# Kernel optimization log

Measured on AMD Instinct MI355X. Metric: run time of the kernel, lower is better.

The kernel has to match this reference:

```python
import jax, jax.numpy as jnp
import numpy as np

B, C, T = 16, 768, 9
S = T * T * T            # 729 tokens
H = 8                    # heads
E = 3                    # experts
HID = C * 4              # expert hidden dim (mult=4)


def setup_inputs() -> dict:
    key = jax.random.key(0)
    ks = jax.random.split(key, 8)
    w = lambda k, sh: (jax.random.normal(k, sh, jnp.float32) * 0.02)
    return {
        "x": jax.random.normal(ks[0], (B, C, T, T, T), jnp.float32),
        "ln_gamma": jnp.ones((C, T, T, T), jnp.float32),
        "ln_beta": jnp.zeros((C, T, T, T), jnp.float32),
        "w_qkv": w(ks[1], (C, 3 * C)),
        "w_out": w(ks[2], (C, C)),
        "w_gate": w(ks[3], (C, E)),
        "b_gate": jnp.zeros((E,), jnp.float32),
        "w1": w(ks[4], (E, C, HID)),
        "b1": jnp.zeros((E, HID), jnp.float32),
        "w2": w(ks[5], (E, HID, C)),
        "b2": jnp.zeros((E, C), jnp.float32),
    }


def reference(x, ln_gamma, ln_beta, w_qkv, w_out, w_gate, b_gate, w1, b1, w2, b2):
    b = x.shape[0]
    # LayerNorm over (C, T, H, W) per batch element, affine params [C,T,T,T]
    mu = jnp.mean(x, axis=(1, 2, 3, 4), keepdims=True)
    var = jnp.var(x, axis=(1, 2, 3, 4), keepdims=True)
    xn = (x - mu) * jax.lax.rsqrt(var + 1e-5) * ln_gamma + ln_beta

    # ---- attention (NOTE: source applies no 1/sqrt(d) scaling) ----
    tok = xn.reshape(b, C, S).transpose(0, 2, 1)                 # [b,s,c]
    qkv = (tok @ w_qkv).reshape(b, S, 3, H, C // H)              # [b,s,3,h,d]
    q = qkv[:, :, 0].transpose(0, 2, 1, 3)                       # [b,h,s,d]
    k = qkv[:, :, 1].transpose(0, 2, 1, 3)
    v = qkv[:, :, 2].transpose(0, 2, 1, 3)
    attn = jax.nn.softmax(jnp.einsum('bhqd,bhkd->bhqk', q, k), axis=-1)
    ctx = jnp.einsum('bhqk,bhkd->bqhd', attn, v).reshape(b, S, C)
    attn_out = (ctx @ w_out).transpose(0, 2, 1).reshape(b, C, T, T, T)
    x2 = x + attn_out                                            # residual (dropout = eval identity)

    # ---- switch-MoE (top-1 gate, all experts computed densely then masked) ----
    tok2 = x2.reshape(b, C, S).transpose(0, 2, 1)                # [b,s,c]
    gate = jax.nn.softmax(tok2 @ w_gate + b_gate, axis=-1)       # [b,s,E]
    mask = jax.nn.one_hot(jnp.argmax(gate, axis=-1), E, dtype=gate.dtype)
    mg = gate * mask
    denom = jnp.sum(mg, axis=0, keepdims=True) + 1e-6            # sum over dim 0, per source
    gate_scores = mg / denom * b                                 # capacity = int(1.0 * b)

    hmid = jax.nn.gelu(jnp.einsum('bsc,ech->bseh', tok2, w1) + b1, approximate=False)
    eout = jnp.einsum('bseh,ehc->bsec', hmid, w2) + b2           # [b,s,E,c]
    moe = jnp.einsum('bse,bsec->bsc', gate_scores, eout)         # weighted mix over experts

    out = x2 + moe.transpose(0, 2, 1).reshape(b, C, T, T, T)
    return out
```

## Files before the change

### kernel.cpp

```cpp
#include <hip/hip_runtime.h>

typedef __bf16 bf16;
typedef __bf16 bf16x4_t __attribute__((ext_vector_type(4)));
typedef __bf16 bf16x8_t __attribute__((ext_vector_type(8)));
typedef float f32x4 __attribute__((ext_vector_type(4)));

#define DEVI __device__ __forceinline__

#define N_B   16
#define N_C   768
#define N_S   729
#define N_TOK 11664
#define TOKP  11776
#define N_H   8
#define N_D   96
#define N_HID 3072
#define MOE_TILES 94
#define GATE_BLOCKS 183

#define OFF_WQKVH 0ull
#define OFF_WQKVL 3538944ull
#define OFF_WOUTH 7077888ull
#define OFF_WOUTL 8257536ull
#define OFF_W1T   9437184ull
#define OFF_W2T   23592960ull
#define OFF_XTOK  37748736ull
#define OFF_R3    73924608ull
#define OFF_TOKH  OFF_R3
#define OFF_TOKL  (OFF_R3 + 18087936ull)
#define OFF_VTH   OFF_R3
#define OFF_VTL   (OFF_R3 + 18087936ull)
#define OFF_T2H   OFF_R3
#define OFF_QKH   110100480ull
#define OFF_QKL   146276352ull
#define OFF_VPH   182452224ull
#define OFF_VPL   200540160ull
#define OFF_CTXH  OFF_VPH
#define OFF_CTXL  OFF_VPL
#define OFF_HMID  OFF_QKH
#define OFF_X2    218628096ull
#define OFF_STATS 254803968ull
#define OFF_DENOM (OFF_STATS + 256ull)
#define OFF_SEL   (OFF_STATS + 16384ull)
#define OFF_PVAL  (OFF_SEL + 65536ull)
#define OFF_GSV   (OFF_PVAL + 65536ull)
#define OFF_PERM  (OFF_GSV + 65536ull)
#define OFF_CNT   (OFF_PERM + 65536ull)

DEVI f32x4 mfma16(bf16x8_t a, bf16x8_t b, f32x4 c) {
  return __builtin_amdgcn_mfma_f32_16x16x32_bf16(a, b, c, 0, 0, 0);
}
DEVI bf16 f2bf(float f) { return (bf16)f; }
DEVI float bf2f(bf16 h) { return (float)h; }
#define GLDS(gp, lp) __builtin_amdgcn_global_load_lds( \
    (__attribute__((address_space(1))) void*)(gp),     \
    (__attribute__((address_space(3))) void*)(lp), 16, 0, 0)

DEVI void xcd_swz(int& bx, int& by) {
  int gx = gridDim.x;
  int nwg = gx * gridDim.y;
  int lin = blockIdx.x + gx * blockIdx.y;
  int xcd = lin & 7, j = lin >> 3;
  int q = nwg >> 3, r = nwg & 7;
  int base = (xcd < r) ? xcd * (q + 1) : r * (q + 1) + (xcd - r) * q;
  int g = base + j;
  by = g / gx;
  bx = g - by * gx;
}

template<bool SPLIT>
__global__ void kxpose(const float* __restrict__ in, bf16* __restrict__ oh,
                       bf16* __restrict__ ol, int R, int Cc) {
  __shared__ float T[32][33];
  int c0 = blockIdx.x * 32, r0 = blockIdx.y * 32;
  int tx = threadIdx.x, ty = threadIdx.y;
#pragma unroll
  for (int i = 0; i < 4; i++)
    T[ty + i * 8][tx] = in[(size_t)(r0 + ty + i * 8) * Cc + c0 + tx];
  __syncthreads();
#pragma unroll
  for (int i = 0; i < 4; i++) {
    float v = T[tx][ty + i * 8];
    size_t o = (size_t)(c0 + ty + i * 8) * R + r0 + tx;
    bf16 hh = f2bf(v);
    oh[o] = hh;
    if constexpr (SPLIT) ol[o] = f2bf(v - bf2f(hh));
  }
}

__global__ __launch_bounds__(256) void ln_stats(const float* __restrict__ x,
                                                double* __restrict__ stats) {
  int b = blockIdx.x >> 7, ch = blockIdx.x & 127;
  const float* xb = x + (size_t)b * 559872;
  int start = ch * 4374;
  float s = 0.f, ss = 0.f;
  for (int i = start + threadIdx.x; i < start + 4374; i += 256) {
    float v = xb[i];
    s += v; ss += v * v;
  }
#pragma unroll
  for (int o = 32; o > 0; o >>= 1) { s += __shfl_down(s, o); ss += __shfl_down(ss, o); }
  __shared__ float rs[4], rss[4];
  int w = threadIdx.x >> 6;
  if ((threadIdx.x & 63) == 0) { rs[w] = s; rss[w] = ss; }
  __syncthreads();
  if (threadIdx.x == 0) {
    atomicAdd(&stats[b * 2 + 0], (double)(rs[0] + rs[1] + rs[2] + rs[3]));
    atomicAdd(&stats[b * 2 + 1], (double)(rss[0] + rss[1] + rss[2] + rss[3]));
  }
}

__global__ void ln_apply(const float* __restrict__ x, const float* __restrict__ g,
                         const float* __restrict__ be, const double* __restrict__ stats,
                         float* __restrict__ xtok, bf16* __restrict__ th, bf16* __restrict__ tl) {
  __shared__ float TN[32][33], TX[32][33];
  int b = blockIdx.z, c0 = blockIdx.y * 32, s0 = blockIdx.x * 32;
  double mu = stats[b * 2] * (1.0 / 559872.0);
  double var = stats[b * 2 + 1] * (1.0 / 559872.0) - mu * mu;
  float rstd = (float)(1.0 / sqrt(var + 1e-5));
  float muf = (float)mu;
  int tx = threadIdx.x, ty = threadIdx.y;
  size_t bo = (size_t)b * 559872;
#pragma unroll
  for (int i = 0; i < 4; i++) {
    int c = c0 + ty + i * 8, s = s0 + tx;
    float v = 0.f, xn = 0.f;
    if (s < N_S) {
      v = x[bo + (size_t)c * 729 + s];
      xn = (v - muf) * rstd * g[(size_t)c * 729 + s] + be[(size_t)c * 729 + s];
    }
    TX[ty + i * 8][tx] = v;
    TN[ty + i * 8][tx] = xn;
  }
  __syncthreads();
#pragma unroll
  for (int i = 0; i < 4; i++) {
    int s = s0 + ty + i * 8;
    if (s < N_S) {
      size_t tok = (size_t)b * 729 + s;
      int c = c0 + tx;
      float xv = TX[tx][ty + i * 8];
      float xn = TN[tx][ty + i * 8];
      xtok[tok * 768 + c] = xv;
      bf16 hh = f2bf(xn);
      th[tok * 768 + c] = hh;
      tl[tok * 768 + c] = f2bf(xn - bf2f(hh));
    }
  }
}

enum { EPI_QKV = 0, EPI_ATTNOUT = 1 };

template<int EPI, bool SPLIT>
__global__ __launch_bounds__(256, 2)
void gemm_k(const bf16* __restrict__ Ah, const bf16* __restrict__ Al,
            const bf16* __restrict__ Bh, const bf16* __restrict__ Bl,
            int M, int N, int K,
            bf16* __restrict__ o0, bf16* __restrict__ o1,
            bf16* __restrict__ o2, bf16* __restrict__ o3,
            float* __restrict__ of, const float* __restrict__ fa) {
  __shared__ __align__(16) bf16 Ash[8192], Bsh[8192];
  __shared__ __align__(16) bf16 Asl[SPLIT ? 8192 : 8], Bsl[SPLIT ? 8192 : 8];
  const int t = threadIdx.x;
  const int lane = t & 63, w = t >> 6;
  const int wr = (w >> 1) << 6, wc = (w & 1) << 6;
  const int lr = lane & 15, lg = lane >> 4;
  int sbx, sby; xcd_swz(sbx, sby);
  const size_t arow = (size_t)sby * 128;
  const size_t brow = (size_t)sbx * 128;
  const int sr = t >> 3;
  const int sg = ((t & 7) ^ (sr & 7)) << 3;
  const bf16* pA = Ah + (arow + sr) * (size_t)K + sg;
  const bf16* pB = Bh + (brow + sr) * (size_t)K + sg;
  const bf16 *pAl = nullptr, *pBl = nullptr;
  if constexpr (SPLIT) {
    pAl = Al + (arow + sr) * (size_t)K + sg;
    pBl = Bl + (brow + sr) * (size_t)K + sg;
  }
  const size_t rstep = (size_t)K << 5;
  f32x4 acc[4][4] = {};
  for (int k0 = 0; k0 < K; k0 += 64) {
    __syncthreads();
#pragma unroll
    for (int c = 0; c < 4; c++) {
      GLDS(pA + c * rstep + k0, &Ash[c * 2048 + t * 8]);
      GLDS(pB + c * rstep + k0, &Bsh[c * 2048 + t * 8]);
      if constexpr (SPLIT) {
        GLDS(pAl + c * rstep + k0, &Asl[c * 2048 + t * 8]);
        GLDS(pBl + c * rstep + k0, &Bsl[c * 2048 + t * 8]);
      }
    }
    asm volatile("s_waitcnt vmcnt(0)" ::: "memory");
    __syncthreads();
#pragma unroll
    for (int kk = 0; kk < 2; kk++) {
      bf16x8_t af[4], bq[4], afl[4], bql[4];
#pragma unroll
      for (int m = 0; m < 4; m++) {
        int row = wr + m * 16 + lr;
        int off = row * 64 + ((((kk << 2) | lg) ^ (row & 7)) << 3);
        af[m] = *(const bf16x8_t*)&Ash[off];
        if constexpr (SPLIT) afl[m] = *(const bf16x8_t*)&Asl[off];
      }
#pragma unroll
      for (int n = 0; n < 4; n++) {
        int row = wc + n * 16 + lr;
        int off = row * 64 + ((((kk << 2) | lg) ^ (row & 7)) << 3);
        bq[n] = *(const bf16x8_t*)&Bsh[off];
        if constexpr (SPLIT) bql[n] = *(const bf16x8_t*)&Bsl[off];
      }
#pragma unroll
      for (int m = 0; m < 4; m++)
#pragma unroll
        for (int n = 0; n < 4; n++) {
          acc[m][n] = mfma16(af[m], bq[n], acc[m][n]);
          if constexpr (SPLIT) {
            acc[m][n] = mfma16(af[m], bql[n], acc[m][n]);
            acc[m][n] = mfma16(afl[m], bq[n], acc[m][n]);
          }
        }
    }
  }
#pragma unroll
  for (int m = 0; m < 4; m++) {
#pragma unroll
    for (int r = 0; r < 4; r++) {
      int gr = (int)arow + wr + m * 16 + lg * 4 + r;
      if (gr >= M) continue;
#pragma unroll
      for (int n = 0; n < 4; n++) {
        int gc = (int)brow + wc + n * 16 + lr;
        float v = acc[m][n][r];
        if constexpr (EPI == EPI_QKV) {
          bf16 hh = f2bf(v);
          bf16 ll = f2bf(v - bf2f(hh));
          if (gc < 1536) {
            size_t oidx = (size_t)gr * 1536 + gc;
            o0[oidx] = hh;
            o1[oidx] = ll;
          } else {
            size_t oidx = (size_t)gr * 768 + (gc - 1536);
            o2[oidx] = hh;
            o3[oidx] = ll;
          }
        } else {
          float x2v = v + fa[(size_t)gr * 768 + gc];
          of[(size_t)gr * 768 + gc] = x2v;
          o0[(size_t)gr * 768 + gc] = f2bf(x2v);
        }
      }
    }
  }
}

__global__ __launch_bounds__(256, 4)
void gemm_moe1(const bf16* __restrict__ Ah, const bf16* __restrict__ W1T,
               const float* __restrict__ b1, const int* __restrict__ perm,
               const int* __restrict__ poff, bf16* __restrict__ hmid) {
  int sbx, sby; xcd_swz(sbx, sby);
  const int arow = sby * 128;
  if (arow >= poff[3]) return;
  const int e = (arow >= poff[1]) + (arow >= poff[2]);
  const bf16* Bh = W1T + (size_t)e * 3072 * 768;
  const float* bias = b1 + e * 3072;
  __shared__ __align__(16) bf16 Ash[8192], Bsh[8192];
  const int t = threadIdx.x;
  const int lane = t & 63, w = t >> 6;
  const int wr = (w >> 1) << 6, wc = (w & 1) << 6;
  const int lr = lane & 15, lg = lane >> 4;
  const size_t brow = (size_t)sbx * 128;
  const int sr = t >> 3;
  const int sg = ((t & 7) ^ (sr & 7)) << 3;
  int ip[4];
#pragma unroll
  for (int c = 0; c < 4; c++) {
    int ii = perm[arow + c * 32 + sr];
    ip[c] = (ii < 0) ? 0 : ii;
  }
  const bf16* pB = Bh + (brow + sr) * 768 + sg;
  const size_t rstep = 768ull << 5;
  f32x4 acc[4][4] = {};
  for (int k0 = 0; k0 < 768; k0 += 64) {
    __syncthreads();
#pragma unroll
    for (int c = 0; c < 4; c++) {
      GLDS(Ah + (size_t)ip[c] * 768 + sg + k0, &Ash[c * 2048 + t * 8]);
      GLDS(pB + c * rstep + k0, &Bsh[c * 2048 + t * 8]);
    }
    asm volatile("s_waitcnt vmcnt(0)" ::: "memory");
    __syncthreads();
#pragma unroll
    for (int kk = 0; kk < 2; kk++) {
      bf16x8_t af[4], bq[4];
#pragma unroll
      for (int m = 0; m < 4; m++) {
        int row = wr + m * 16 + lr;
        af[m] = *(const bf16x8_t*)&Ash[row * 64 + ((((kk << 2) | lg) ^ (row & 7)) << 3)];
      }
#pragma unroll
      for (int n = 0; n < 4; n++) {
        int row = wc + n * 16 + lr;
        bq[n] = *(const bf16x8_t*)&Bsh[row * 64 + ((((kk << 2) | lg) ^ (row & 7)) << 3)];
      }
#pragma unroll
      for (int m = 0; m < 4; m++)
#pragma unroll
        for (int n = 0; n < 4; n++)
          acc[m][n] = mfma16(af[m], bq[n], acc[m][n]);
    }
  }
#pragma unroll
  for (int m = 0; m < 4; m++)
#pragma unroll
    for (int r = 0; r < 4; r++) {
      int gr = arow + wr + m * 16 + lg * 4 + r;
#pragma unroll
      for (int n = 0; n < 4; n++) {
        int gc = (int)brow + wc + n * 16 + lr;
        float z = acc[m][n][r] + bias[gc];
        float gl = 0.5f * z * (1.f + erff(z * 0.7071067811865476f));
        hmid[(size_t)gr * 3072 + gc] = f2bf(gl);
      }
    }
}

__global__ __launch_bounds__(256, 4)
void gemm_moe2(const bf16* __restrict__ hmid, const bf16* __restrict__ W2T,
               const float* __restrict__ b2, const int* __restrict__ perm,
               const int* __restrict__ poff, const float* __restrict__ gsv,
               float* __restrict__ moe) {
  int sbx, sby; xcd_swz(sbx, sby);
  const int arow = sby * 128;
  if (arow >= poff[3]) return;
  const int e = (arow >= poff[1]) + (arow >= poff[2]);
  const bf16* Bh = W2T + (size_t)e * 768 * 3072;
  const float* bias = b2 + e * 768;
  __shared__ __align__(16) bf16 Ash[8192], Bsh[8192];
  const int t = threadIdx.x;
  const int lane = t & 63, w = t >> 6;
  const int wr = (w >> 1) << 6, wc = (w & 1) << 6;
  const int lr = lane & 15, lg = lane >> 4;
  const size_t brow = (size_t)sbx * 128;
  const int sr = t >> 3;
  const int sg = ((t & 7) ^ (sr & 7)) << 3;
  const bf16* pA = hmid + (size_t)(arow + sr) * 3072 + sg;
  const bf16* pB = Bh + (brow + sr) * 3072 + sg;
  const size_t rstep = 3072ull << 5;
  f32x4 acc[4][4] = {};
  for (int k0 = 0; k0 < 3072; k0 += 64) {
    __syncthreads();
#pragma unroll
    for (int c = 0; c < 4; c++) {
      GLDS(pA + c * rstep + k0, &Ash[c * 2048 + t * 8]);
      GLDS(pB + c * rstep + k0, &Bsh[c * 2048 + t * 8]);
    }
    asm volatile("s_waitcnt vmcnt(0)" ::: "memory");
    __syncthreads();
#pragma unroll
    for (int kk = 0; kk < 2; kk++) {
      bf16x8_t af[4], bq[4];
#pragma unroll
      for (int m = 0; m < 4; m++) {
        int row = wr + m * 16 + lr;
        af[m] = *(const bf16x8_t*)&Ash[row * 64 + ((((kk << 2) | lg) ^ (row & 7)) << 3)];
      }
#pragma unroll
      for (int n = 0; n < 4; n++) {
        int row = wc + n * 16 + lr;
        bq[n] = *(const bf16x8_t*)&Bsh[row * 64 + ((((kk << 2) | lg) ^ (row & 7)) << 3)];
      }
#pragma unroll
      for (int m = 0; m < 4; m++)
#pragma unroll
        for (int n = 0; n < 4; n++)
          acc[m][n] = mfma16(af[m], bq[n], acc[m][n]);
    }
  }
#pragma unroll
  for (int m = 0; m < 4; m++)
#pragma unroll
    for (int r = 0; r < 4; r++) {
      int gr = arow + wr + m * 16 + lg * 4 + r;
      int tok = perm[gr];
      if (tok < 0) continue;
      float gv = gsv[tok];
#pragma unroll
      for (int n = 0; n < 4; n++) {
        int gc = (int)brow + wc + n * 16 + lr;
        moe[(size_t)tok * 768 + gc] = (acc[m][n][r] + bias[gc]) * gv;
      }
    }
}

__global__ __launch_bounds__(256) void repack_v(const bf16* __restrict__ vph,
    const bf16* __restrict__ vpl, bf16* __restrict__ vth, bf16* __restrict__ vtl) {
  __shared__ bf16 Lh[96][40], Ll[96][40];
  int t = threadIdx.x;
  int bh = blockIdx.y, b = bh >> 3, h = bh & 7;
  int s0 = blockIdx.x * 32;
  for (int v = t; v < 384; v += 256) {
    int e0 = v * 8;
    int r = e0 / 96;
    int c = e0 - r * 96;
    size_t src = ((size_t)b * 729 + s0 + r) * 768 + h * 96 + c;
    bf16x8_t xh = *(const bf16x8_t*)&vph[src];
    bf16x8_t xl = *(const bf16x8_t*)&vpl[src];
    bool ok = (s0 + r) < N_S;
#pragma unroll
    for (int j = 0; j < 8; j++) {
      Lh[c + j][r] = ok ? xh[j] : f2bf(0.f);
      Ll[c + j][r] = ok ? xl[j] : f2bf(0.f);
    }
  }
  __syncthreads();
  for (int vv = t; vv < 768; vv += 256) {
    int e0 = vv * 4;
    int d = e0 >> 5, sl = e0 & 31;
    bf16x4_t ohv, olv;
#pragma unroll
    for (int j = 0; j < 4; j++) { ohv[j] = Lh[d][sl + j]; olv[j] = Ll[d][sl + j]; }
    size_t dst = (size_t)bh * (96ull * 736ull) + (size_t)d * 736 + s0 + sl;
    *(bf16x4_t*)&vth[dst] = ohv;
    *(bf16x4_t*)&vtl[dst] = olv;
  }
}

DEVI int pslot(int w, int s) { return ((s >> 9) << 11) + (w << 9) + (s & 511); }

__global__ __launch_bounds__(256, 3)
void attn(const bf16* __restrict__ qkh, const bf16* __restrict__ qkl,
          const bf16* __restrict__ vth, const bf16* __restrict__ vtl,
          bf16* __restrict__ ch, bf16* __restrict__ cl) {
  __shared__ bf16 Ksh[6144], Ksl[6144], Vsh[6144], Vsl[6144];
  const int t = threadIdx.x, lane = t & 63, w = t >> 6;
  const int lr = lane & 15, lg = lane >> 4;
  int sbx, sby; xcd_swz(sbx, sby);
  const int bh = sby, b = bh >> 3, h = bh & 7;
  const int q0 = sbx * 64;
  const size_t tokbase = (size_t)b * 729;
  const int qr = w * 16 + lr;
  const size_t qrow = (tokbase + q0 + qr) * 1536ull + (size_t)h * 96;
  bf16x8_t qh[3], ql[3];
#pragma unroll
  for (int ks = 0; ks < 3; ks++) {
    qh[ks] = *(const bf16x8_t*)&qkh[qrow + ks * 32 + lg * 8];
    ql[ks] = *(const bf16x8_t*)&qkl[qrow + ks * 32 + lg * 8];
  }

  auto loadK = [&](int kt) {
    const int kv0 = kt * 64;
#pragma unroll
    for (int chk = 0; chk < 3; chk++) {
      int kv = t >> 2, dg = t & 3;
      int sdg = dg ^ (kv & 3);
      size_t ksrc = (tokbase + kv0 + kv) * 1536ull + 768ull + (size_t)h * 96 + chk * 32 + (sdg << 3);
      int ldsoff = chk * 2048 + t * 8;
      GLDS(qkh + ksrc, &Ksh[ldsoff]);
      GLDS(qkl + ksrc, &Ksl[ldsoff]);
    }
  };
  auto loadV = [&](int kt) {
    const int kv0 = kt * 64;
#pragma unroll
    for (int chk = 0; chk < 3; chk++) {
      int ldsoff = chk * 2048 + t * 8;
      int d = ldsoff >> 6;
      int grp = (ldsoff >> 3) & 7;
      int sg = grp ^ (d & 7);
      size_t vsrc = (size_t)bh * (96ull * 736ull) + (size_t)d * 736 + kv0 + (sg << 3);
      GLDS(vth + vsrc, &Vsh[ldsoff]);
      GLDS(vtl + vsrc, &Vsl[ldsoff]);
    }
  };

  float mrow[4] = {-1e30f, -1e30f, -1e30f, -1e30f};
  float lpart[4] = {0.f, 0.f, 0.f, 0.f};
  f32x4 octx[6] = {};

  loadK(0);
  asm volatile("s_waitcnt vmcnt(0)" ::: "memory");
  __syncthreads();
  loadV(0);

  for (int kt = 0; kt < 12; kt++) {
    const int kv0 = kt * 64;
    f32x4 sc[4];
    __builtin_amdgcn_s_setprio(1);
#pragma unroll
    for (int cf = 0; cf < 4; cf++) {
      f32x4 a = {0.f, 0.f, 0.f, 0.f};
      int kvrow = cf * 16 + lr;
#pragma unroll
      for (int ks = 0; ks < 3; ks++) {
        int slot = ks * 2048 + kvrow * 32 + ((lg ^ (kvrow & 3)) << 3);
        bf16x8_t kh = *(const bf16x8_t*)&Ksh[slot];
        bf16x8_t kl = *(const bf16x8_t*)&Ksl[slot];
        a = mfma16(qh[ks], kh, a);
        a = mfma16(qh[ks], kl, a);
        a = mfma16(ql[ks], kh, a);
      }
      if (kv0 + kvrow >= N_S) { a[0] = -1e30f; a[1] = -1e30f; a[2] = -1e30f; a[3] = -1e30f; }
      sc[cf] = a;
    }
    __builtin_amdgcn_s_setprio(0);
    float lmax[4];
#pragma unroll
    for (int r = 0; r < 4; r++)
      lmax[r] = fmaxf(fmaxf(sc[0][r], sc[1][r]), fmaxf(sc[2][r], sc[3][r]));
    bool ok = (lmax[0] <= mrow[0] + 8.f) && (lmax[1] <= mrow[1] + 8.f) &&
              (lmax[2] <= mrow[2] + 8.f) && (lmax[3] <= mrow[3] + 8.f);
    if (!__all(ok)) {
      float escv[4];
#pragma unroll
      for (int r = 0; r < 4; r++) {
        float a = lmax[r];
#pragma unroll
        for (int o = 1; o < 16; o <<= 1) a = fmaxf(a, __shfl_xor(a, o));
        float mn = fmaxf(mrow[r], a);
        escv[r] = __expf(mrow[r] - mn);
        mrow[r] = mn;
        lpart[r] *= escv[r];
      }
#pragma unroll
      for (int df = 0; df < 6; df++)
#pragma unroll
        for (int r = 0; r < 4; r++) octx[df][r] *= escv[r];
    }
#pragma unroll
    for (int cf = 0; cf < 4; cf++)
#pragma unroll
      for (int r = 0; r < 4; r++) {
        float p = __expf(sc[cf][r] - mrow[r]);
        sc[cf][r] = p;
        lpart[r] += p;
      }
    asm volatile("s_waitcnt vmcnt(0)" ::: "memory");
    __syncthreads();
#pragma unroll
    for (int cf = 0; cf < 4; cf++)
#pragma unroll
      for (int r = 0; r < 4; r++) {
        int qloc = lg * 4 + r;
        int kvg = (cf << 1) | (lr >> 3);
        int xw = (qloc ^ (qloc >> 2)) & 7;
        int slot = qloc * 64 + (((kvg ^ xw) << 3) | (lr & 7));
        float p = sc[cf][r];
        bf16 hp = f2bf(p);
        int ps = pslot(w, slot);
        Ksh[ps] = hp;
        Ksl[ps] = f2bf(p - bf2f(hp));
      }
    asm volatile("s_waitcnt lgkmcnt(0)" ::: "memory");
    __builtin_amdgcn_sched_barrier(0);
    bf16x8_t pah[2], pal[2];
#pragma unroll
    for (int ks = 0; ks < 2; ks++) {
      int xr = (lr ^ (lr >> 2)) & 7;
      int slot = lr * 64 + ((((ks << 2) | lg) ^ xr) << 3);
      int ps = pslot(w, slot);
      pah[ks] = *(const bf16x8_t*)&Ksh[ps];
      pal[ks] = *(const bf16x8_t*)&Ksl[ps];
    }
    asm volatile("s_waitcnt lgkmcnt(0)" ::: "memory");
    __builtin_amdgcn_sched_barrier(0);
    if (kt < 11) loadK(kt + 1);
    __builtin_amdgcn_s_setprio(1);
#pragma unroll
    for (int df = 0; df < 6; df++) {
      int dd = df * 16 + lr;
#pragma unroll
      for (int ks = 0; ks < 2; ks++) {
        int slot = dd * 64 + ((((ks << 2) | lg) ^ (dd & 7)) << 3);
        bf16x8_t vh = *(const bf16x8_t*)&Vsh[slot];
        bf16x8_t vl = *(const bf16x8_t*)&Vsl[slot];
        octx[df] = mfma16(pah[ks], vh, octx[df]);
        octx[df] = mfma16(pah[ks], vl, octx[df]);
        octx[df] = mfma16(pal[ks], vh, octx[df]);
      }
    }
    __builtin_amdgcn_s_setprio(0);
    if (kt < 11) {
      asm volatile("s_waitcnt vmcnt(0)" ::: "memory");
      __syncthreads();
      loadV(kt + 1);
    }
  }
  float lrow[4];
#pragma unroll
  for (int r = 0; r < 4; r++) {
    float a = lpart[r];
#pragma unroll
    for (int o = 1; o < 16; o <<= 1) a += __shfl_xor(a, o);
    lrow[r] = a;
  }
#pragma unroll
  for (int r = 0; r < 4; r++) {
    int qloc = w * 16 + lg * 4 + r;
    if (q0 + qloc >= N_S) continue;
    size_t orow = (tokbase + q0 + qloc) * 768ull + (size_t)h * 96;
    float inv = 1.f / lrow[r];
#pragma unroll
    for (int df = 0; df < 6; df++) {
      float v = octx[df][r] * inv;
      bf16 hh = f2bf(v);
      ch[orow + df * 16 + lr] = hh;
      cl[orow + df * 16 + lr] = f2bf(v - bf2f(hh));
    }
  }
}

__global__ __launch_bounds__(256) void gate_k(const float* __restrict__ x2,
    const float* __restrict__ wg, const float* __restrict__ bg,
    int* __restrict__ sel, float* __restrict__ pval, float* __restrict__ denom,
    int* __restrict__ cnt) {
  int lane = threadIdx.x & 63, w = threadIdx.x >> 6;
  float wv[12][3];
#pragma unroll
  for (int j = 0; j < 12; j++) {
    int c = lane + j * 64;
    const float* wgc = wg + c * 3;
    wv[j][0] = wgc[0]; wv[j][1] = wgc[1]; wv[j][2] = wgc[2];
  }
  float bg0 = bg[0], bg1 = bg[1], bg2 = bg[2];
  int cloc0 = 0, cloc1 = 0, cloc2 = 0;
  int base_tok = (blockIdx.x * 4 + w) * 16;
  for (int it = 0; it < 16; it++) {
    int tok = base_tok + it;
    if (tok >= N_TOK) break;
    const float* row = x2 + (size_t)tok * 768;
    double a0 = 0, a1 = 0, a2 = 0;
#pragma unroll
    for (int j = 0; j < 12; j++) {
      float xv = row[lane + j * 64];
      a0 += (double)(xv * wv[j][0]);
      a1 += (double)(xv * wv[j][1]);
      a2 += (double)(xv * wv[j][2]);
    }
#pragma unroll
    for (int o = 32; o > 0; o >>= 1) {
      a0 += __shfl_down(a0, o);
      a1 += __shfl_down(a1, o);
      a2 += __shfl_down(a2, o);
    }
    if (lane == 0) {
      float g0 = (float)a0 + bg0, g1 = (float)a1 + bg1, g2 = (float)a2 + bg2;
      float mx = fmaxf(g0, fmaxf(g1, g2));
      float e0 = __expf(g0 - mx), e1 = __expf(g1 - mx), e2 = __expf(g2 - mx);
      float inv = 1.f / (e0 + e1 + e2);
      int am = 0; float pm = e0;
      if (e1 > pm) { pm = e1; am = 1; }
      if (e2 > pm) { pm = e2; am = 2; }
      float p = pm * inv;
      sel[tok] = am;
      pval[tok] = p;
      int s = tok - (tok / 729) * 729;
      atomicAdd(&denom[s * 3 + am], p);
      cloc0 += (am == 0); cloc1 += (am == 1); cloc2 += (am == 2);
    }
  }
  __shared__ int bc[3];
  if (threadIdx.x == 0) { bc[0] = 0; bc[1] = 0; bc[2] = 0; }
  __syncthreads();
  if (lane == 0) {
    if (cloc0) atomicAdd(&bc[0], cloc0);
    if (cloc1) atomicAdd(&bc[1], cloc1);
    if (cloc2) atomicAdd(&bc[2], cloc2);
  }
  __syncthreads();
  if (threadIdx.x < 3 && bc[threadIdx.x]) atomicAdd(&cnt[threadIdx.x], bc[threadIdx.x]);
}

__global__ void moe_scan(const int* __restrict__ cnt, int* __restrict__ poff) {
  int p1 = (cnt[0] + 127) & ~127;
  int p2 = p1 + ((cnt[1] + 127) & ~127);
  int p3 = p2 + ((cnt[2] + 127) & ~127);
  poff[0] = 0; poff[1] = p1; poff[2] = p2; poff[3] = p3;
}

__global__ __launch_bounds__(256) void moe_scatter(const int* __restrict__ sel,
                            const float* __restrict__ pval,
                            const float* __restrict__ denom, const int* __restrict__ poff,
                            int* __restrict__ cur, int* __restrict__ perm,
                            float* __restrict__ gsv) {
  int tok = blockIdx.x * 256 + threadIdx.x;
  int lane = threadIdx.x & 63, w = threadIdx.x >> 6;
  bool valid = tok < N_TOK;
  int e = valid ? sel[tok] : -1;
  if (valid) {
    int s = tok - (tok / 729) * 729;
    gsv[tok] = pval[tok] * 16.f / (denom[s * 3 + e] + 1e-6f);
  }
  unsigned long long m0 = __ballot(e == 0);
  unsigned long long m1 = __ballot(e == 1);
  unsigned long long m2 = __ballot(e == 2);
  __shared__ int wcnt[4][3], wbase[4][3];
  if (lane == 0) {
    wcnt[w][0] = __popcll(m0);
    wcnt[w][1] = __popcll(m1);
    wcnt[w][2] = __popcll(m2);
  }
  __syncthreads();
  if (threadIdx.x < 3) {
    int x = threadIdx.x;
    int c0 = wcnt[0][x], c1 = wcnt[1][x], c2 = wcnt[2][x], c3 = wcnt[3][x];
    int base = atomicAdd(&cur[x], c0 + c1 + c2 + c3);
    wbase[0][x] = base;
    wbase[1][x] = base + c0;
    wbase[2][x] = base + c0 + c1;
    wbase[3][x] = base + c0 + c1 + c2;
  }
  __syncthreads();
  if (valid) {
    unsigned long long lt = (lane == 0) ? 0ull : ((~0ull) >> (64 - lane));
    unsigned long long me = (e == 0) ? m0 : (e == 1) ? m1 : m2;
    int pos = wbase[w][e] + __popcll(me & lt);
    perm[poff[e] + pos] = tok;
  }
}

__global__ void final_k(const float* __restrict__ x2, const float* __restrict__ moe,
                        float* __restrict__ out) {
  __shared__ float L[32][33];
  int b = blockIdx.z, c0 = blockIdx.y * 32, s0 = blockIdx.x * 32;
  int tx = threadIdx.x, ty = threadIdx.y;
#pragma unroll
  for (int i = 0; i < 4; i++) {
    int s = s0 + ty + i * 8;
    float v = 0.f;
    if (s < N_S) {
      size_t tok = (size_t)b * 729 + s;
      v = x2[tok * 768 + c0 + tx] + moe[tok * 768 + c0 + tx];
    }
    L[ty + i * 8][tx] = v;
  }
  __syncthreads();
#pragma unroll
  for (int i = 0; i < 4; i++) {
    int s = s0 + tx;
    int c = c0 + ty + i * 8;
    if (s < N_S) out[((size_t)b * 768 + c) * 729 + s] = L[tx][ty + i * 8];
  }
}

extern "C" void kernel_launch(void* const* d_in, const int* in_sizes, int n_in,
                              void* d_out, int out_size, void* d_ws, size_t ws_size,
                              hipStream_t stream) {
  (void)in_sizes; (void)n_in; (void)out_size; (void)ws_size;
  const float* x     = (const float*)d_in[0];
  const float* lng   = (const float*)d_in[1];
  const float* lnb   = (const float*)d_in[2];
  const float* wqkv  = (const float*)d_in[3];
  const float* wout  = (const float*)d_in[4];
  const float* wgate = (const float*)d_in[5];
  const float* bgate = (const float*)d_in[6];
  const float* w1    = (const float*)d_in[7];
  const float* b1    = (const float*)d_in[8];
  const float* w2    = (const float*)d_in[9];
  const float* b2    = (const float*)d_in[10];
  float* out = (float*)d_out;
  char* ws = (char*)d_ws;

  bf16* WQKVH = (bf16*)(ws + OFF_WQKVH);
  bf16* WQKVL = (bf16*)(ws + OFF_WQKVL);
  bf16* WOUTH = (bf16*)(ws + OFF_WOUTH);
  bf16* WOUTL = (bf16*)(ws + OFF_WOUTL);
  bf16* W1T   = (bf16*)(ws + OFF_W1T);
  bf16* W2T   = (bf16*)(ws + OFF_W2T);
  float* XTOK = (float*)(ws + OFF_XTOK);
  float* MOE  = (float*)(ws + OFF_XTOK);
  bf16* TOKH  = (bf16*)(ws + OFF_TOKH);
  bf16* TOKL  = (bf16*)(ws + OFF_TOKL);
  bf16* VTH   = (bf16*)(ws + OFF_VTH);
  bf16* VTL   = (bf16*)(ws + OFF_VTL);
  bf16* T2H   = (bf16*)(ws + OFF_T2H);
  bf16* QKH   = (bf16*)(ws + OFF_QKH);
  bf16* QKL   = (bf16*)(ws + OFF_QKL);
  bf16* VPH   = (bf16*)(ws + OFF_VPH);
  bf16* VPL   = (bf16*)(ws + OFF_VPL);
  bf16* CTXH  = (bf16*)(ws + OFF_CTXH);
  bf16* CTXL  = (bf16*)(ws + OFF_CTXL);
  bf16* HMID  = (bf16*)(ws + OFF_HMID);
  float* X2   = (float*)(ws + OFF_X2);
  double* STATS = (double*)(ws + OFF_STATS);
  float* DENOM  = (float*)(ws + OFF_DENOM);
  int*   SEL    = (int*)(ws + OFF_SEL);
  float* PVAL   = (float*)(ws + OFF_PVAL);
  float* GSV    = (float*)(ws + OFF_GSV);
  int*   PERM   = (int*)(ws + OFF_PERM);
  int*   CNT    = (int*)(ws + OFF_CNT);
  int*   POFF   = CNT + 4;
  int*   CUR    = CNT + 8;

  hipMemsetAsync(ws + OFF_STATS, 0, 16384, stream);
  hipMemsetAsync(ws + OFF_CNT, 0, 64, stream);
  hipMemsetAsync(ws + OFF_PERM, 0xFF, MOE_TILES * 128 * 4, stream);

  dim3 tb(32, 8);
  kxpose<true><<<dim3(72, 24), tb, 0, stream>>>(wqkv, WQKVH, WQKVL, 768, 2304);
  kxpose<true><<<dim3(24, 24), tb, 0, stream>>>(wout, WOUTH, WOUTL, 768, 768);
  for (int e = 0; e < 3; e++) {
    kxpose<false><<<dim3(96, 24), tb, 0, stream>>>(w1 + (size_t)e * 768 * 3072,
        W1T + (size_t)e * 3072 * 768, nullptr, 768, 3072);
    kxpose<false><<<dim3(24, 96), tb, 0, stream>>>(w2 + (size_t)e * 3072 * 768,
        W2T + (size_t)e * 768 * 3072, nullptr, 3072, 768);
  }
  ln_stats<<<2048, 256, 0, stream>>>(x, STATS);
  ln_apply<<<dim3(23, 24, 16), tb, 0, stream>>>(x, lng, lnb, STATS, XTOK, TOKH, TOKL);
  gemm_k<EPI_QKV, true><<<dim3(18, 92), 256, 0, stream>>>(
      TOKH, TOKL, WQKVH, WQKVL, N_TOK, 2304, 768,
      QKH, QKL, VPH, VPL, nullptr, nullptr);
  repack_v<<<dim3(23, 128), 256, 0, stream>>>(VPH, VPL, VTH, VTL);
  attn<<<dim3(12, 128), 256, 0, stream>>>(QKH, QKL, VTH, VTL, CTXH, CTXL);
  gemm_k<EPI_ATTNOUT, true><<<dim3(6, 92), 256, 0, stream>>>(
      CTXH, CTXL, WOUTH, WOUTL, N_TOK, 768, 768,
      T2H, nullptr, nullptr, nullptr, X2, XTOK);
  gate_k<<<GATE_BLOCKS, 256, 0, stream>>>(X2, wgate, bgate, SEL, PVAL, DENOM, CNT);
  moe_scan<<<1, 1, 0, stream>>>(CNT, POFF);
  moe_scatter<<<46, 256, 0, stream>>>(SEL, PVAL, DENOM, POFF, CUR, PERM, GSV);
  gemm_moe1<<<dim3(24, MOE_TILES), 256, 0, stream>>>(T2H, W1T, b1, PERM, POFF, HMID);
  gemm_moe2<<<dim3(6, MOE_TILES), 256, 0, stream>>>(HMID, W2T, b2, PERM, POFF, GSV, MOE);
  final_k<<<dim3(23, 24, 16), tb, 0, stream>>>(X2, MOE, out);
}
```

Before: 656.3 us.

## Double-buffer LDS tiles in MoE expert GEMMs to overlap loads with MFMA

```diff
diff --git a/kernel.cpp b/kernel.cpp
--- a/kernel.cpp
+++ b/kernel.cpp
@@ -253,7 +253,7 @@
   }
 }
 
-__global__ __launch_bounds__(256, 4)
+__global__ __launch_bounds__(256, 2)
 void gemm_moe1(const bf16* __restrict__ Ah, const bf16* __restrict__ W1T,
                const float* __restrict__ b1, const int* __restrict__ perm,
                const int* __restrict__ poff, bf16* __restrict__ hmid) {
@@ -263,7 +263,7 @@
   const int e = (arow >= poff[1]) + (arow >= poff[2]);
   const bf16* Bh = W1T + (size_t)e * 3072 * 768;
   const float* bias = b1 + e * 3072;
-  __shared__ __align__(16) bf16 Ash[8192], Bsh[8192];
+  __shared__ __align__(16) bf16 Ash[2][8192], Bsh[2][8192];
   const int t = threadIdx.x;
   const int lane = t & 63, w = t >> 6;
   const int wr = (w >> 1) << 6, wc = (w & 1) << 6;
@@ -279,28 +279,32 @@
   }
   const bf16* pB = Bh + (brow + sr) * 768 + sg;
   const size_t rstep = 768ull << 5;
+  auto stage = [&](int buf, int k0) {
+#pragma unroll
+    for (int c = 0; c < 4; c++) {
+      GLDS(Ah + (size_t)ip[c] * 768 + sg + k0, &Ash[buf][c * 2048 + t * 8]);
+      GLDS(pB + c * rstep + k0, &Bsh[buf][c * 2048 + t * 8]);
+    }
+  };
   f32x4 acc[4][4] = {};
+  stage(0, 0);
+  asm volatile("s_waitcnt vmcnt(0)" ::: "memory");
+  __syncthreads();
+  int cur = 0;
   for (int k0 = 0; k0 < 768; k0 += 64) {
-    __syncthreads();
-#pragma unroll
-    for (int c = 0; c < 4; c++) {
-      GLDS(Ah + (size_t)ip[c] * 768 + sg + k0, &Ash[c * 2048 + t * 8]);
-      GLDS(pB + c * rstep + k0, &Bsh[c * 2048 + t * 8]);
-    }
-    asm volatile("s_waitcnt vmcnt(0)" ::: "memory");
-    __syncthreads();
+    if (k0 + 64 < 768) stage(cur ^ 1, k0 + 64);
 #pragma unroll
     for (int kk = 0; kk < 2; kk++) {
       bf16x8_t af[4], bq[4];
 #pragma unroll
       for (int m = 0; m < 4; m++) {
         int row = wr + m * 16 + lr;
-        af[m] = *(const bf16x8_t*)&Ash[row * 64 + ((((kk << 2) | lg) ^ (row & 7)) << 3)];
+        af[m] = *(const bf16x8_t*)&Ash[cur][row * 64 + ((((kk << 2) | lg) ^ (row & 7)) << 3)];
       }
 #pragma unroll
       for (int n = 0; n < 4; n++) {
         int row = wc + n * 16 + lr;
-        bq[n] = *(const bf16x8_t*)&Bsh[row * 64 + ((((kk << 2) | lg) ^ (row & 7)) << 3)];
+        bq[n] = *(const bf16x8_t*)&Bsh[cur][row * 64 + ((((kk << 2) | lg) ^ (row & 7)) << 3)];
       }
 #pragma unroll
       for (int m = 0; m < 4; m++)
@@ -308,6 +312,8 @@
         for (int n = 0; n < 4; n++)
           acc[m][n] = mfma16(af[m], bq[n], acc[m][n]);
     }
+    __syncthreads();
+    cur ^= 1;
   }
 #pragma unroll
   for (int m = 0; m < 4; m++)
@@ -324,7 +330,7 @@
     }
 }
 
-__global__ __launch_bounds__(256, 4)
+__global__ __launch_bounds__(256, 2)
 void gemm_moe2(const bf16* __restrict__ hmid, const bf16* __restrict__ W2T,
                const float* __restrict__ b2, const int* __restrict__ perm,
                const int* __restrict__ poff, const float* __restrict__ gsv,
@@ -335,7 +341,7 @@
   const int e = (arow >= poff[1]) + (arow >= poff[2]);
   const bf16* Bh = W2T + (size_t)e * 768 * 3072;
   const float* bias = b2 + e * 768;
-  __shared__ __align__(16) bf16 Ash[8192], Bsh[8192];
+  __shared__ __align__(16) bf16 Ash[2][8192], Bsh[2][8192];
   const int t = threadIdx.x;
   const int lane = t & 63, w = t >> 6;
   const int wr = (w >> 1) << 6, wc = (w & 1) << 6;
@@ -346,28 +352,32 @@
   const bf16* pA = hmid + (size_t)(arow + sr) * 3072 + sg;
   const bf16* pB = Bh + (brow + sr) * 3072 + sg;
   const size_t rstep = 3072ull << 5;
+  auto stage = [&](int buf, int k0) {
+#pragma unroll
+    for (int c = 0; c < 4; c++) {
+      GLDS(pA + c * rstep + k0, &Ash[buf][c * 2048 + t * 8]);
+      GLDS(pB + c * rstep + k0, &Bsh[buf][c * 2048 + t * 8]);
+    }
+  };
   f32x4 acc[4][4] = {};
+  stage(0, 0);
+  asm volatile("s_waitcnt vmcnt(0)" ::: "memory");
+  __syncthreads();
+  int cur = 0;
   for (int k0 = 0; k0 < 3072; k0 += 64) {
-    __syncthreads();
-#pragma unroll
-    for (int c = 0; c < 4; c++) {
-      GLDS(pA + c * rstep + k0, &Ash[c * 2048 + t * 8]);
-      GLDS(pB + c * rstep + k0, &Bsh[c * 2048 + t * 8]);
-    }
-    asm volatile("s_waitcnt vmcnt(0)" ::: "memory");
-    __syncthreads();
+    if (k0 + 64 < 3072) stage(cur ^ 1, k0 + 64);
 #pragma unroll
     for (int kk = 0; kk < 2; kk++) {
       bf16x8_t af[4], bq[4];
 #pragma unroll
       for (int m = 0; m < 4; m++) {
         int row = wr + m * 16 + lr;
-        af[m] = *(const bf16x8_t*)&Ash[row * 64 + ((((kk << 2) | lg) ^ (row & 7)) << 3)];
+        af[m] = *(const bf16x8_t*)&Ash[cur][row * 64 + ((((kk << 2) | lg) ^ (row & 7)) << 3)];
       }
 #pragma unroll
       for (int n = 0; n < 4; n++) {
         int row = wc + n * 16 + lr;
-        bq[n] = *(const bf16x8_t*)&Bsh[row * 64 + ((((kk << 2) | lg) ^ (row & 7)) << 3)];
+        bq[n] = *(const bf16x8_t*)&Bsh[cur][row * 64 + ((((kk << 2) | lg) ^ (row & 7)) << 3)];
       }
 #pragma unroll
       for (int m = 0; m < 4; m++)
@@ -375,6 +385,8 @@
         for (int n = 0; n < 4; n++)
           acc[m][n] = mfma16(af[m], bq[n], acc[m][n]);
     }
+    __syncthreads();
+    cur ^= 1;
   }
 #pragma unroll
   for (int m = 0; m < 4; m++)
```

Measured after the change: 726.8 us. 10.7% more time.
